# Kernel optimization log

Hardware: AMD Instinct MI355X
Metric: run time of the kernel (lower is better)

## Reference

```python
import jax, jax.numpy as jnp
import numpy as np

HEADS = 8
EMBED = 512


def setup_inputs() -> dict:
    key = jax.random.key(0)
    ks = jax.random.split(key, 9)
    N, KL, QL, S = 4, 512, 32, 64
    D = EMBED // HEADS
    return {
        "values": jax.random.normal(ks[0], (N, KL, EMBED), jnp.float32),
        "keys": jax.random.normal(ks[1], (N, KL, EMBED), jnp.float32),
        "query": jax.random.normal(ks[2], (N, QL, S, EMBED), jnp.float32),
        "mask": jax.random.randint(ks[3], (N, 1, 1, KL, 1), 0, 2, jnp.int32),
        "Wv": jax.random.normal(ks[4], (D, D), jnp.float32) * 0.05,
        "Wk": jax.random.normal(ks[5], (D, D), jnp.float32) * 0.05,
        "Wq": jax.random.normal(ks[6], (D, D), jnp.float32) * 0.05,
        "Wo": jax.random.normal(ks[7], (EMBED, EMBED), jnp.float32) * 0.05,
        "bo": jax.random.normal(ks[8], (EMBED,), jnp.float32) * 0.05,
    }


def reference(values, keys, query, mask, Wv, Wk, Wq, Wo, bo):
    N, KL, E = keys.shape
    QL, S = query.shape[1], query.shape[2]
    H = HEADS
    D = E // H
    # split heads, then per-head linear (weights shared across heads, torch y = x @ W.T)
    v = jnp.einsum('nkhd,ed->nkhe', values.reshape(N, KL, H, D), Wv)
    k = jnp.einsum('nkhd,ed->nkhe', keys.reshape(N, KL, H, D), Wk)
    q = jnp.einsum('nqshd,ed->nqshe', query.reshape(N, QL, S, H, D), Wq)
    # energy: [N, H, QL, KL, S]
    energy = jnp.einsum('nqshd,nkhd->nhqks', q, k)
    energy = jnp.where(mask == 0, jnp.float32(-1e20), energy)
    scale = jnp.float32(E ** 0.5)
    attention = jax.nn.softmax(energy / scale, axis=3)  # softmax over key axis
    out = jnp.einsum('nhqks,nkhd->nqshd', attention, v).reshape(N, QL, S, E)
    return out @ Wo.T + bo
```

## Files before the change

kernel.cpp:

```cpp
#include <hip/hip_runtime.h>
#include <math.h>


typedef __bf16 bf16;
typedef __attribute__((ext_vector_type(8))) __bf16 bf16x8;
typedef __attribute__((ext_vector_type(4))) __bf16 bf16x4;
typedef __attribute__((ext_vector_type(4))) float f32x4;

#define LA 72
#define QSCALE (0.044194173824159216f * 1.4426950408889634f)
#define MASK_BIAS -64.0f

__global__ __launch_bounds__(256) void wcvt(const float* __restrict__ Wq,
                                            const float* __restrict__ Wk,
                                            const float* __restrict__ Wv,
                                            const float* __restrict__ Wo,
                                            bf16* __restrict__ Wq_bf,
                                            bf16* __restrict__ Wk_bf,
                                            bf16* __restrict__ Wv_bf,
                                            bf16* __restrict__ Wo_bf) {
    int t = blockIdx.x * 256 + threadIdx.x;
    if (t < 262144) Wo_bf[t] = (bf16)Wo[t];
    if (t < 4096) {
        Wq_bf[t] = (bf16)(Wq[t] * QSCALE);
        Wk_bf[t] = (bf16)Wk[t];
        Wv_bf[t] = (bf16)Wv[t];
    }
}

__global__ __launch_bounds__(128, 2) void kv_proj(const float* __restrict__ keys,
                                                  const float* __restrict__ values,
                                                  const bf16* __restrict__ Wk_bf,
                                                  const bf16* __restrict__ Wv_bf,
                                                  bf16* __restrict__ Kp,
                                                  bf16* __restrict__ Vt) {
    __shared__ bf16 Xk[64 * LA];
    __shared__ bf16 Xv[64 * LA];
    int t = threadIdx.x;
    int nh = blockIdx.x >> 3, kt = blockIdx.x & 7;
    int n = nh >> 3, h = nh & 7;
    int kl0 = kt * 64;
#pragma unroll
    for (int i = 0; i < 8; ++i) {
        int f = t + i * 128;
        int row = f >> 4, c4 = f & 15;
        float4 a = *(const float4*)(keys + ((long)n * 512 + kl0 + row) * 512 + h * 64 + c4 * 4);
        float4 b = *(const float4*)(values + ((long)n * 512 + kl0 + row) * 512 + h * 64 + c4 * 4);
        bf16x4 ak = {(bf16)a.x, (bf16)a.y, (bf16)a.z, (bf16)a.w};
        bf16x4 bv = {(bf16)b.x, (bf16)b.y, (bf16)b.z, (bf16)b.w};
        *(bf16x4*)&Xk[row * LA + c4 * 4] = ak;
        *(bf16x4*)&Xv[row * LA + c4 * 4] = bv;
    }
    __syncthreads();
    int w = t >> 6, quad = (t >> 4) & 3, c16 = t & 15;
    {
        f32x4 acc[2][4];
#pragma unroll
        for (int mb = 0; mb < 2; ++mb)
#pragma unroll
            for (int nb = 0; nb < 4; ++nb) acc[mb][nb] = (f32x4){0.f, 0.f, 0.f, 0.f};
#pragma unroll
        for (int kc = 0; kc < 2; ++kc) {
            bf16x8 a0 = *(const bf16x8*)&Xk[(32 * w + c16) * LA + 32 * kc + quad * 8];
            bf16x8 a1 = *(const bf16x8*)&Xk[(32 * w + 16 + c16) * LA + 32 * kc + quad * 8];
#pragma unroll
            for (int nb = 0; nb < 4; ++nb) {
                bf16x8 b = *(const bf16x8*)(Wk_bf + (16 * nb + c16) * 64 + 32 * kc + quad * 8);
                acc[0][nb] = __builtin_amdgcn_mfma_f32_16x16x32_bf16(a0, b, acc[0][nb], 0, 0, 0);
                acc[1][nb] = __builtin_amdgcn_mfma_f32_16x16x32_bf16(a1, b, acc[1][nb], 0, 0, 0);
            }
        }
#pragma unroll
        for (int mb = 0; mb < 2; ++mb)
#pragma unroll
            for (int nb = 0; nb < 4; ++nb)
#pragma unroll
                for (int r = 0; r < 4; ++r)
                    Kp[((long)nh * 512 + kl0 + 32 * w + 16 * mb + quad * 4 + r) * 64 + 16 * nb + c16] =
                        (bf16)acc[mb][nb][r];
    }
    {
        f32x4 acc[2][4];
#pragma unroll
        for (int mb = 0; mb < 2; ++mb)
#pragma unroll
            for (int nb = 0; nb < 4; ++nb) acc[mb][nb] = (f32x4){0.f, 0.f, 0.f, 0.f};
#pragma unroll
        for (int kc = 0; kc < 2; ++kc) {
            bf16x8 a0 = *(const bf16x8*)(Wv_bf + (32 * w + c16) * 64 + 32 * kc + quad * 8);
            bf16x8 a1 = *(const bf16x8*)(Wv_bf + (32 * w + 16 + c16) * 64 + 32 * kc + quad * 8);
#pragma unroll
            for (int nb = 0; nb < 4; ++nb) {
                bf16x8 b = *(const bf16x8*)&Xv[(16 * nb + c16) * LA + 32 * kc + quad * 8];
                acc[0][nb] = __builtin_amdgcn_mfma_f32_16x16x32_bf16(a0, b, acc[0][nb], 0, 0, 0);
                acc[1][nb] = __builtin_amdgcn_mfma_f32_16x16x32_bf16(a1, b, acc[1][nb], 0, 0, 0);
            }
        }
#pragma unroll
        for (int mb = 0; mb < 2; ++mb)
#pragma unroll
            for (int nb = 0; nb < 4; ++nb)
#pragma unroll
                for (int r = 0; r < 4; ++r)
                    Vt[((long)nh * 64 + 32 * w + 16 * mb + quad * 4 + r) * 512 + kl0 + 16 * nb + c16] =
                        (bf16)acc[mb][nb][r];
    }
}

__global__ __launch_bounds__(256, 2) void attn(const float* __restrict__ query,
                                               const bf16* __restrict__ Wq_bf,
                                               const bf16* __restrict__ Kp,
                                               const bf16* __restrict__ Vtg,
                                               const int* __restrict__ mask,
                                               bf16* __restrict__ AO) {
    __shared__ bf16 Xq[128 * LA];
    __shared__ bf16 Qt[128 * LA];
    __shared__ bf16 Kt[64 * LA];
    __shared__ bf16 Vs[64 * LA];
    __shared__ bf16 St[128 * LA];
    __shared__ float Mb[64];
    int t = threadIdx.x;
    int qt = blockIdx.x & 15;
    int nh = blockIdx.x >> 4;
    int n = nh >> 3, h = nh & 7;
    int r0 = qt * 128;
    int w = t >> 6, quad = (t >> 4) & 3, c16 = t & 15;

#pragma unroll
    for (int i = 0; i < 8; ++i) {
        int f = t + i * 256;
        int row = f >> 4, c4 = f & 15;
        float4 a = *(const float4*)(query + ((long)n * 2048 + r0 + row) * 512 + h * 64 + c4 * 4);
        bf16x4 v = {(bf16)a.x, (bf16)a.y, (bf16)a.z, (bf16)a.w};
        *(bf16x4*)&Xq[row * LA + c4 * 4] = v;
    }
    __syncthreads();
    {
        f32x4 qa[2][4];
#pragma unroll
        for (int mb = 0; mb < 2; ++mb)
#pragma unroll
            for (int nb = 0; nb < 4; ++nb) qa[mb][nb] = (f32x4){0.f, 0.f, 0.f, 0.f};
#pragma unroll
        for (int kc = 0; kc < 2; ++kc) {
            bf16x8 a0 = *(const bf16x8*)&Xq[(32 * w + c16) * LA + 32 * kc + quad * 8];
            bf16x8 a1 = *(const bf16x8*)&Xq[(32 * w + 16 + c16) * LA + 32 * kc + quad * 8];
#pragma unroll
            for (int nb = 0; nb < 4; ++nb) {
                bf16x8 b = *(const bf16x8*)(Wq_bf + (16 * nb + c16) * 64 + 32 * kc + quad * 8);
                qa[0][nb] = __builtin_amdgcn_mfma_f32_16x16x32_bf16(a0, b, qa[0][nb], 0, 0, 0);
                qa[1][nb] = __builtin_amdgcn_mfma_f32_16x16x32_bf16(a1, b, qa[1][nb], 0, 0, 0);
            }
        }
#pragma unroll
        for (int mb = 0; mb < 2; ++mb)
#pragma unroll
            for (int nb = 0; nb < 4; ++nb)
#pragma unroll
                for (int r = 0; r < 4; ++r)
                    Qt[(32 * w + 16 * mb + quad * 4 + r) * LA + 16 * nb + c16] = (bf16)qa[mb][nb][r];
    }

    f32x4 oacc[4][2];
#pragma unroll
    for (int mb = 0; mb < 4; ++mb)
#pragma unroll
        for (int nb = 0; nb < 2; ++nb) oacc[mb][nb] = (f32x4){0.f, 0.f, 0.f, 0.f};
    float ps[2] = {0.f, 0.f};
    const bf16* Kb = Kp + (long)nh * 512 * 64;
    const bf16* Vb = Vtg + (long)nh * 64 * 512;

    for (int kt = 0; kt < 8; ++kt) {
        __syncthreads();
#pragma unroll
        for (int i = 0; i < 2; ++i) {
            int f = t + i * 256;
            int row = f >> 3, c = f & 7;
            *(bf16x8*)&Kt[row * LA + c * 8] = *(const bf16x8*)(Kb + ((long)kt * 64 + row) * 64 + c * 8);
            *(bf16x8*)&Vs[row * LA + c * 8] = *(const bf16x8*)(Vb + (long)row * 512 + kt * 64 + c * 8);
        }
        if (t < 64) Mb[t] = mask[n * 512 + kt * 64 + t] ? 0.f : MASK_BIAS;
        __syncthreads();
        f32x4 sc[4][2];
#pragma unroll
        for (int mb = 0; mb < 4; ++mb) {
            f32x4 bias = *(const f32x4*)&Mb[16 * mb + quad * 4];
            sc[mb][0] = bias;
            sc[mb][1] = bias;
        }
#pragma unroll
        for (int kc = 0; kc < 2; ++kc) {
            bf16x8 ka[4];
#pragma unroll
            for (int mb = 0; mb < 4; ++mb)
                ka[mb] = *(const bf16x8*)&Kt[(16 * mb + c16) * LA + 32 * kc + quad * 8];
#pragma unroll
            for (int nb = 0; nb < 2; ++nb) {
                bf16x8 qb = *(const bf16x8*)&Qt[(32 * w + 16 * nb + c16) * LA + 32 * kc + quad * 8];
#pragma unroll
                for (int mb = 0; mb < 4; ++mb)
                    sc[mb][nb] = __builtin_amdgcn_mfma_f32_16x16x32_bf16(ka[mb], qb, sc[mb][nb], 0, 0, 0);
            }
        }
#pragma unroll
        for (int mb = 0; mb < 4; ++mb)
#pragma unroll
            for (int nb = 0; nb < 2; ++nb) {
                float p0 = exp2f(sc[mb][nb][0]);
                float p1 = exp2f(sc[mb][nb][1]);
                float p2 = exp2f(sc[mb][nb][2]);
                float p3 = exp2f(sc[mb][nb][3]);
                ps[nb] += (p0 + p1) + (p2 + p3);
                bf16x4 pb = {(bf16)p0, (bf16)p1, (bf16)p2, (bf16)p3};
                *(bf16x4*)&St[(32 * w + 16 * nb + c16) * LA + 16 * mb + quad * 4] = pb;
            }
#pragma unroll
        for (int kc = 0; kc < 2; ++kc) {
            bf16x8 va[4];
#pragma unroll
            for (int mb = 0; mb < 4; ++mb)
                va[mb] = *(const bf16x8*)&Vs[(16 * mb + c16) * LA + 32 * kc + quad * 8];
#pragma unroll
            for (int nb = 0; nb < 2; ++nb) {
                bf16x8 pb = *(const bf16x8*)&St[(32 * w + 16 * nb + c16) * LA + 32 * kc + quad * 8];
#pragma unroll
                for (int mb = 0; mb < 4; ++mb)
                    oacc[mb][nb] = __builtin_amdgcn_mfma_f32_16x16x32_bf16(va[mb], pb, oacc[mb][nb], 0, 0, 0);
            }
        }
    }
#pragma unroll
    for (int nb = 0; nb < 2; ++nb) {
        ps[nb] += __shfl_xor(ps[nb], 16);
        ps[nb] += __shfl_xor(ps[nb], 32);
    }
    float il[2] = {1.0f / ps[0], 1.0f / ps[1]};
#pragma unroll
    for (int mb = 0; mb < 4; ++mb)
#pragma unroll
        for (int nb = 0; nb < 2; ++nb) {
            int row_g = r0 + 32 * w + 16 * nb + c16;
            int d = 16 * mb + quad * 4;
            bf16x4 o = {(bf16)(oacc[mb][nb][0] * il[nb]), (bf16)(oacc[mb][nb][1] * il[nb]),
                        (bf16)(oacc[mb][nb][2] * il[nb]), (bf16)(oacc[mb][nb][3] * il[nb])};
            *(bf16x4*)(AO + ((long)n * 2048 + row_g) * 512 + h * 64 + d) = o;
        }
}

__global__ __launch_bounds__(256, 2) void out_gemm(const bf16* __restrict__ A,
                                                   const bf16* __restrict__ Wo_bf,
                                                   const float* __restrict__ bo,
                                                   float* __restrict__ C) {
    __shared__ bf16 At[128 * LA];
    __shared__ bf16 Bt[64 * LA];
    int t = threadIdx.x;
    int br = blockIdx.x >> 3, bc = blockIdx.x & 7;
    int r0 = br * 128, c0 = bc * 64;
    int w = t >> 6, quad = (t >> 4) & 3, c16 = t & 15;
    f32x4 acc[2][4];
#pragma unroll
    for (int mb = 0; mb < 2; ++mb)
#pragma unroll
        for (int nb = 0; nb < 4; ++nb) acc[mb][nb] = (f32x4){0.f, 0.f, 0.f, 0.f};
    for (int k0 = 0; k0 < 512; k0 += 64) {
        __syncthreads();
#pragma unroll
        for (int i = 0; i < 4; ++i) {
            int f = t + i * 256;
            int row = f >> 3, c = f & 7;
            *(bf16x8*)&At[row * LA + c * 8] = *(const bf16x8*)(A + (long)(r0 + row) * 512 + k0 + c * 8);
        }
#pragma unroll
        for (int i = 0; i < 2; ++i) {
            int f = t + i * 256;
            int row = f >> 3, c = f & 7;
            *(bf16x8*)&Bt[row * LA + c * 8] = *(const bf16x8*)(Wo_bf + (long)(c0 + row) * 512 + k0 + c * 8);
        }
        __syncthreads();
#pragma unroll
        for (int kc = 0; kc < 2; ++kc) {
            bf16x8 a0 = *(const bf16x8*)&At[(32 * w + c16) * LA + 32 * kc + quad * 8];
            bf16x8 a1 = *(const bf16x8*)&At[(32 * w + 16 + c16) * LA + 32 * kc + quad * 8];
#pragma unroll
            for (int nb = 0; nb < 4; ++nb) {
                bf16x8 b = *(const bf16x8*)&Bt[(16 * nb + c16) * LA + 32 * kc + quad * 8];
                acc[0][nb] = __builtin_amdgcn_mfma_f32_16x16x32_bf16(a0, b, acc[0][nb], 0, 0, 0);
                acc[1][nb] = __builtin_amdgcn_mfma_f32_16x16x32_bf16(a1, b, acc[1][nb], 0, 0, 0);
            }
        }
    }
#pragma unroll
    for (int mb = 0; mb < 2; ++mb)
#pragma unroll
        for (int nb = 0; nb < 4; ++nb) {
            float bias = bo[c0 + 16 * nb + c16];
#pragma unroll
            for (int r = 0; r < 4; ++r)
                C[(long)(r0 + 32 * w + 16 * mb + quad * 4 + r) * 512 + c0 + 16 * nb + c16] =
                    acc[mb][nb][r] + bias;
        }
}

extern "C" void kernel_launch(void* const* d_in, const int* in_sizes, int n_in,
                              void* d_out, int out_size, void* d_ws, size_t ws_size,
                              hipStream_t stream) {
    const float* values = (const float*)d_in[0];
    const float* keys   = (const float*)d_in[1];
    const float* query  = (const float*)d_in[2];
    const int*   maskp  = (const int*)d_in[3];
    const float* Wv     = (const float*)d_in[4];
    const float* Wk     = (const float*)d_in[5];
    const float* Wq     = (const float*)d_in[6];
    const float* Wo     = (const float*)d_in[7];
    const float* bo     = (const float*)d_in[8];
    float* out = (float*)d_out;

    bf16* ws = (bf16*)d_ws;
    bf16* Kp    = ws;
    bf16* Vt    = Kp + 1048576;
    bf16* AO    = Vt + 1048576;
    bf16* Wq_bf = AO + 4194304;
    bf16* Wk_bf = Wq_bf + 4096;
    bf16* Wv_bf = Wk_bf + 4096;
    bf16* Wo_bf = Wv_bf + 4096;

    wcvt<<<dim3(1024), dim3(256), 0, stream>>>(Wq, Wk, Wv, Wo, Wq_bf, Wk_bf, Wv_bf, Wo_bf);
    kv_proj<<<dim3(256), dim3(128), 0, stream>>>(keys, values, Wk_bf, Wv_bf, Kp, Vt);
    attn<<<dim3(512), dim3(256), 0, stream>>>(query, Wq_bf, Kp, Vt, maskp, AO);
    out_gemm<<<dim3(512), dim3(256), 0, stream>>>(AO, Wo_bf, bo, out);
}
```

Before: 127.5 us.

## Drop weight-conversion kernel, prefetch K/V tiles, reuse LDS, remap block order

The separate weight-conversion launch is removed. Each kernel now converts its fp32 weights to bf16 in registers, and Wq is scaled on load. kv_proj uses 256 threads so the K and V projections run on separate warps in parallel. attn and out_gemm prefetch the next K/V/mask or A/Wo tile into registers while the current tile is computed. attn also shares one LDS buffer between Xq and the probability tile, lowers padding to 68 and raises occupancy to 3 blocks. Block index orderings change for L2 locality, in exchange for redundant weight conversion in every block and more register pressure.

Measured after the change: 126.0 us. Within noise of the previous version (-1.2%).

```diff
diff --git a/kernel.cpp b/kernel.cpp
--- a/kernel.cpp
+++ b/kernel.cpp
@@ -7,53 +7,47 @@
 typedef __attribute__((ext_vector_type(4))) __bf16 bf16x4;
 typedef __attribute__((ext_vector_type(4))) float f32x4;
 
-#define LA 72
+#define LW 68
+#define LS 72
 #define QSCALE (0.044194173824159216f * 1.4426950408889634f)
 #define MASK_BIAS -64.0f
 
-__global__ __launch_bounds__(256) void wcvt(const float* __restrict__ Wq,
-                                            const float* __restrict__ Wk,
-                                            const float* __restrict__ Wv,
-                                            const float* __restrict__ Wo,
-                                            bf16* __restrict__ Wq_bf,
-                                            bf16* __restrict__ Wk_bf,
-                                            bf16* __restrict__ Wv_bf,
-                                            bf16* __restrict__ Wo_bf) {
-    int t = blockIdx.x * 256 + threadIdx.x;
-    if (t < 262144) Wo_bf[t] = (bf16)Wo[t];
-    if (t < 4096) {
-        Wq_bf[t] = (bf16)(Wq[t] * QSCALE);
-        Wk_bf[t] = (bf16)Wk[t];
-        Wv_bf[t] = (bf16)Wv[t];
-    }
-}
-
-__global__ __launch_bounds__(128, 2) void kv_proj(const float* __restrict__ keys,
+__device__ __forceinline__ bf16x8 cvt8(const float* p, float s) {
+    float4 x0 = *(const float4*)p;
+    float4 x1 = *(const float4*)(p + 4);
+    bf16x8 r = {(bf16)(x0.x * s), (bf16)(x0.y * s), (bf16)(x0.z * s), (bf16)(x0.w * s),
+                (bf16)(x1.x * s), (bf16)(x1.y * s), (bf16)(x1.z * s), (bf16)(x1.w * s)};
+    return r;
+}
+
+__global__ __launch_bounds__(256, 2) void kv_proj(const float* __restrict__ keys,
                                                   const float* __restrict__ values,
-                                                  const bf16* __restrict__ Wk_bf,
-                                                  const bf16* __restrict__ Wv_bf,
+                                                  const float* __restrict__ Wk,
+                                                  const float* __restrict__ Wv,
                                                   bf16* __restrict__ Kp,
                                                   bf16* __restrict__ Vt) {
-    __shared__ bf16 Xk[64 * LA];
-    __shared__ bf16 Xv[64 * LA];
+    __shared__ bf16 Xk[64 * LW];
+    __shared__ bf16 Xv[64 * LW];
     int t = threadIdx.x;
     int nh = blockIdx.x >> 3, kt = blockIdx.x & 7;
-    int n = nh >> 3, h = nh & 7;
-    int kl0 = kt * 64;
-#pragma unroll
-    for (int i = 0; i < 8; ++i) {
-        int f = t + i * 128;
-        int row = f >> 4, c4 = f & 15;
+    int n = nh >> 3, h = nh & 7, kl0 = kt * 64;
+    int w = t >> 6, quad = (t >> 4) & 3, c16 = t & 15;
+#pragma unroll
+    for (int i = 0; i < 4; ++i) {
+        int f = t + i * 256, row = f >> 4, c4 = f & 15;
         float4 a = *(const float4*)(keys + ((long)n * 512 + kl0 + row) * 512 + h * 64 + c4 * 4);
         float4 b = *(const float4*)(values + ((long)n * 512 + kl0 + row) * 512 + h * 64 + c4 * 4);
-        bf16x4 ak = {(bf16)a.x, (bf16)a.y, (bf16)a.z, (bf16)a.w};
-        bf16x4 bv = {(bf16)b.x, (bf16)b.y, (bf16)b.z, (bf16)b.w};
-        *(bf16x4*)&Xk[row * LA + c4 * 4] = ak;
-        *(bf16x4*)&Xv[row * LA + c4 * 4] = bv;
+        *(bf16x4*)&Xk[row * LW + c4 * 4] = (bf16x4){(bf16)a.x, (bf16)a.y, (bf16)a.z, (bf16)a.w};
+        *(bf16x4*)&Xv[row * LW + c4 * 4] = (bf16x4){(bf16)b.x, (bf16)b.y, (bf16)b.z, (bf16)b.w};
     }
     __syncthreads();
-    int w = t >> 6, quad = (t >> 4) & 3, c16 = t & 15;
-    {
+    if (w < 2) {
+        bf16x8 wf[8];
+#pragma unroll
+        for (int nb = 0; nb < 4; ++nb)
+#pragma unroll
+            for (int kc = 0; kc < 2; ++kc)
+                wf[nb * 2 + kc] = cvt8(Wk + (16 * nb + c16) * 64 + 32 * kc + quad * 8, 1.0f);
         f32x4 acc[2][4];
 #pragma unroll
         for (int mb = 0; mb < 2; ++mb)
@@ -61,13 +55,12 @@
             for (int nb = 0; nb < 4; ++nb) acc[mb][nb] = (f32x4){0.f, 0.f, 0.f, 0.f};
 #pragma unroll
         for (int kc = 0; kc < 2; ++kc) {
-            bf16x8 a0 = *(const bf16x8*)&Xk[(32 * w + c16) * LA + 32 * kc + quad * 8];
-            bf16x8 a1 = *(const bf16x8*)&Xk[(32 * w + 16 + c16) * LA + 32 * kc + quad * 8];
+            bf16x8 a0 = *(const bf16x8*)&Xk[(32 * w + c16) * LW + 32 * kc + quad * 8];
+            bf16x8 a1 = *(const bf16x8*)&Xk[(32 * w + 16 + c16) * LW + 32 * kc + quad * 8];
 #pragma unroll
             for (int nb = 0; nb < 4; ++nb) {
-                bf16x8 b = *(const bf16x8*)(Wk_bf + (16 * nb + c16) * 64 + 32 * kc + quad * 8);
-                acc[0][nb] = __builtin_amdgcn_mfma_f32_16x16x32_bf16(a0, b, acc[0][nb], 0, 0, 0);
-                acc[1][nb] = __builtin_amdgcn_mfma_f32_16x16x32_bf16(a1, b, acc[1][nb], 0, 0, 0);
+                acc[0][nb] = __builtin_amdgcn_mfma_f32_16x16x32_bf16(a0, wf[nb * 2 + kc], acc[0][nb], 0, 0, 0);
+                acc[1][nb] = __builtin_amdgcn_mfma_f32_16x16x32_bf16(a1, wf[nb * 2 + kc], acc[1][nb], 0, 0, 0);
             }
         }
 #pragma unroll
@@ -78,8 +71,14 @@
                 for (int r = 0; r < 4; ++r)
                     Kp[((long)nh * 512 + kl0 + 32 * w + 16 * mb + quad * 4 + r) * 64 + 16 * nb + c16] =
                         (bf16)acc[mb][nb][r];
-    }
-    {
+    } else {
+        int w2 = w - 2;
+        bf16x8 af[4];
+#pragma unroll
+        for (int mb = 0; mb < 2; ++mb)
+#pragma unroll
+            for (int kc = 0; kc < 2; ++kc)
+                af[mb * 2 + kc] = cvt8(Wv + (32 * w2 + 16 * mb + c16) * 64 + 32 * kc + quad * 8, 1.0f);
         f32x4 acc[2][4];
 #pragma unroll
         for (int mb = 0; mb < 2; ++mb)
@@ -87,13 +86,11 @@
             for (int nb = 0; nb < 4; ++nb) acc[mb][nb] = (f32x4){0.f, 0.f, 0.f, 0.f};
 #pragma unroll
         for (int kc = 0; kc < 2; ++kc) {
-            bf16x8 a0 = *(const bf16x8*)(Wv_bf + (32 * w + c16) * 64 + 32 * kc + quad * 8);
-            bf16x8 a1 = *(const bf16x8*)(Wv_bf + (32 * w + 16 + c16) * 64 + 32 * kc + quad * 8);
 #pragma unroll
             for (int nb = 0; nb < 4; ++nb) {
-                bf16x8 b = *(const bf16x8*)&Xv[(16 * nb + c16) * LA + 32 * kc + quad * 8];
-                acc[0][nb] = __builtin_amdgcn_mfma_f32_16x16x32_bf16(a0, b, acc[0][nb], 0, 0, 0);
-                acc[1][nb] = __builtin_amdgcn_mfma_f32_16x16x32_bf16(a1, b, acc[1][nb], 0, 0, 0);
+                bf16x8 b = *(const bf16x8*)&Xv[(16 * nb + c16) * LW + 32 * kc + quad * 8];
+                acc[0][nb] = __builtin_amdgcn_mfma_f32_16x16x32_bf16(af[kc], b, acc[0][nb], 0, 0, 0);
+                acc[1][nb] = __builtin_amdgcn_mfma_f32_16x16x32_bf16(af[2 + kc], b, acc[1][nb], 0, 0, 0);
             }
         }
 #pragma unroll
@@ -102,37 +99,51 @@
             for (int nb = 0; nb < 4; ++nb)
 #pragma unroll
                 for (int r = 0; r < 4; ++r)
-                    Vt[((long)nh * 64 + 32 * w + 16 * mb + quad * 4 + r) * 512 + kl0 + 16 * nb + c16] =
+                    Vt[((long)nh * 64 + 32 * w2 + 16 * mb + quad * 4 + r) * 512 + kl0 + 16 * nb + c16] =
                         (bf16)acc[mb][nb][r];
     }
 }
 
-__global__ __launch_bounds__(256, 2) void attn(const float* __restrict__ query,
-                                               const bf16* __restrict__ Wq_bf,
+__global__ __launch_bounds__(256, 3) void attn(const float* __restrict__ query,
+                                               const float* __restrict__ Wq,
                                                const bf16* __restrict__ Kp,
                                                const bf16* __restrict__ Vtg,
                                                const int* __restrict__ mask,
                                                bf16* __restrict__ AO) {
-    __shared__ bf16 Xq[128 * LA];
-    __shared__ bf16 Qt[128 * LA];
-    __shared__ bf16 Kt[64 * LA];
-    __shared__ bf16 Vs[64 * LA];
-    __shared__ bf16 St[128 * LA];
+    __shared__ bf16 SX[128 * LS];
+    __shared__ bf16 Qt[128 * LW];
+    __shared__ bf16 Kt[64 * LW];
+    __shared__ bf16 Vs[64 * LW];
     __shared__ float Mb[64];
     int t = threadIdx.x;
-    int qt = blockIdx.x & 15;
-    int nh = blockIdx.x >> 4;
+    int nh = blockIdx.x & 31, qtile = blockIdx.x >> 5;
     int n = nh >> 3, h = nh & 7;
-    int r0 = qt * 128;
+    int r0 = qtile * 128;
     int w = t >> 6, quad = (t >> 4) & 3, c16 = t & 15;
+    const bf16* Kb = Kp + (long)nh * 512 * 64;
+    const bf16* Vb = Vtg + (long)nh * 64 * 512;
+
+    int prow0 = t >> 3, pcol0 = t & 7;
+    int prow1 = (t + 256) >> 3, pcol1 = t & 7;
+    bf16x8 pk0 = *(const bf16x8*)(Kb + (long)prow0 * 64 + pcol0 * 8);
+    bf16x8 pk1 = *(const bf16x8*)(Kb + (long)prow1 * 64 + pcol1 * 8);
+    bf16x8 pv0 = *(const bf16x8*)(Vb + (long)prow0 * 512 + pcol0 * 8);
+    bf16x8 pv1 = *(const bf16x8*)(Vb + (long)prow1 * 512 + pcol1 * 8);
+    float mnext = 0.f;
+    if (t < 64) mnext = mask[n * 512 + t] ? 0.f : MASK_BIAS;
+
+    bf16x8 wf[8];
+#pragma unroll
+    for (int nb = 0; nb < 4; ++nb)
+#pragma unroll
+        for (int kc = 0; kc < 2; ++kc)
+            wf[nb * 2 + kc] = cvt8(Wq + (16 * nb + c16) * 64 + 32 * kc + quad * 8, QSCALE);
 
 #pragma unroll
     for (int i = 0; i < 8; ++i) {
-        int f = t + i * 256;
-        int row = f >> 4, c4 = f & 15;
+        int f = t + i * 256, row = f >> 4, c4 = f & 15;
         float4 a = *(const float4*)(query + ((long)n * 2048 + r0 + row) * 512 + h * 64 + c4 * 4);
-        bf16x4 v = {(bf16)a.x, (bf16)a.y, (bf16)a.z, (bf16)a.w};
-        *(bf16x4*)&Xq[row * LA + c4 * 4] = v;
+        *(bf16x4*)&SX[row * LS + c4 * 4] = (bf16x4){(bf16)a.x, (bf16)a.y, (bf16)a.z, (bf16)a.w};
     }
     __syncthreads();
     {
@@ -143,13 +154,12 @@
             for (int nb = 0; nb < 4; ++nb) qa[mb][nb] = (f32x4){0.f, 0.f, 0.f, 0.f};
 #pragma unroll
         for (int kc = 0; kc < 2; ++kc) {
-            bf16x8 a0 = *(const bf16x8*)&Xq[(32 * w + c16) * LA + 32 * kc + quad * 8];
-            bf16x8 a1 = *(const bf16x8*)&Xq[(32 * w + 16 + c16) * LA + 32 * kc + quad * 8];
+            bf16x8 a0 = *(const bf16x8*)&SX[(32 * w + c16) * LS + 32 * kc + quad * 8];
+            bf16x8 a1 = *(const bf16x8*)&SX[(32 * w + 16 + c16) * LS + 32 * kc + quad * 8];
 #pragma unroll
             for (int nb = 0; nb < 4; ++nb) {
-                bf16x8 b = *(const bf16x8*)(Wq_bf + (16 * nb + c16) * 64 + 32 * kc + quad * 8);
-                qa[0][nb] = __builtin_amdgcn_mfma_f32_16x16x32_bf16(a0, b, qa[0][nb], 0, 0, 0);
-                qa[1][nb] = __builtin_amdgcn_mfma_f32_16x16x32_bf16(a1, b, qa[1][nb], 0, 0, 0);
+                qa[0][nb] = __builtin_amdgcn_mfma_f32_16x16x32_bf16(a0, wf[nb * 2 + kc], qa[0][nb], 0, 0, 0);
+                qa[1][nb] = __builtin_amdgcn_mfma_f32_16x16x32_bf16(a1, wf[nb * 2 + kc], qa[1][nb], 0, 0, 0);
             }
         }
 #pragma unroll
@@ -158,7 +168,7 @@
             for (int nb = 0; nb < 4; ++nb)
 #pragma unroll
                 for (int r = 0; r < 4; ++r)
-                    Qt[(32 * w + 16 * mb + quad * 4 + r) * LA + 16 * nb + c16] = (bf16)qa[mb][nb][r];
+                    Qt[(32 * w + 16 * mb + quad * 4 + r) * LW + 16 * nb + c16] = (bf16)qa[mb][nb][r];
     }
 
     f32x4 oacc[4][2];
@@ -167,20 +177,24 @@
 #pragma unroll
         for (int nb = 0; nb < 2; ++nb) oacc[mb][nb] = (f32x4){0.f, 0.f, 0.f, 0.f};
     float ps[2] = {0.f, 0.f};
-    const bf16* Kb = Kp + (long)nh * 512 * 64;
-    const bf16* Vb = Vtg + (long)nh * 64 * 512;
 
     for (int kt = 0; kt < 8; ++kt) {
+        if (kt) __syncthreads();
+        *(bf16x8*)&Kt[prow0 * LW + pcol0 * 8] = pk0;
+        *(bf16x8*)&Kt[prow1 * LW + pcol1 * 8] = pk1;
+        *(bf16x8*)&Vs[prow0 * LW + pcol0 * 8] = pv0;
+        *(bf16x8*)&Vs[prow1 * LW + pcol1 * 8] = pv1;
+        if (t < 64) Mb[t] = mnext;
         __syncthreads();
-#pragma unroll
-        for (int i = 0; i < 2; ++i) {
-            int f = t + i * 256;
-            int row = f >> 3, c = f & 7;
-            *(bf16x8*)&Kt[row * LA + c * 8] = *(const bf16x8*)(Kb + ((long)kt * 64 + row) * 64 + c * 8);
-            *(bf16x8*)&Vs[row * LA + c * 8] = *(const bf16x8*)(Vb + (long)row * 512 + kt * 64 + c * 8);
-        }
-        if (t < 64) Mb[t] = mask[n * 512 + kt * 64 + t] ? 0.f : MASK_BIAS;
-        __syncthreads();
+        if (kt < 7) {
+            const bf16* Kn = Kb + (long)(kt + 1) * 64 * 64;
+            const bf16* Vn = Vb + (kt + 1) * 64;
+            pk0 = *(const bf16x8*)(Kn + (long)prow0 * 64 + pcol0 * 8);
+            pk1 = *(const bf16x8*)(Kn + (long)prow1 * 64 + pcol1 * 8);
+            pv0 = *(const bf16x8*)(Vn + (long)prow0 * 512 + pcol0 * 8);
+            pv1 = *(const bf16x8*)(Vn + (long)prow1 * 512 + pcol1 * 8);
+            if (t < 64) mnext = mask[n * 512 + (kt + 1) * 64 + t] ? 0.f : MASK_BIAS;
+        }
         f32x4 sc[4][2];
 #pragma unroll
         for (int mb = 0; mb < 4; ++mb) {
@@ -193,10 +207,10 @@
             bf16x8 ka[4];
 #pragma unroll
             for (int mb = 0; mb < 4; ++mb)
-                ka[mb] = *(const bf16x8*)&Kt[(16 * mb + c16) * LA + 32 * kc + quad * 8];
+                ka[mb] = *(const bf16x8*)&Kt[(16 * mb + c16) * LW + 32 * kc + quad * 8];
 #pragma unroll
             for (int nb = 0; nb < 2; ++nb) {
-                bf16x8 qb = *(const bf16x8*)&Qt[(32 * w + 16 * nb + c16) * LA + 32 * kc + quad * 8];
+                bf16x8 qb = *(const bf16x8*)&Qt[(32 * w + 16 * nb + c16) * LW + 32 * kc + quad * 8];
 #pragma unroll
                 for (int mb = 0; mb < 4; ++mb)
                     sc[mb][nb] = __builtin_amdgcn_mfma_f32_16x16x32_bf16(ka[mb], qb, sc[mb][nb], 0, 0, 0);
@@ -211,18 +225,18 @@
                 float p2 = exp2f(sc[mb][nb][2]);
                 float p3 = exp2f(sc[mb][nb][3]);
                 ps[nb] += (p0 + p1) + (p2 + p3);
-                bf16x4 pb = {(bf16)p0, (bf16)p1, (bf16)p2, (bf16)p3};
-                *(bf16x4*)&St[(32 * w + 16 * nb + c16) * LA + 16 * mb + quad * 4] = pb;
+                *(bf16x4*)&SX[(32 * w + 16 * nb + c16) * LS + 16 * mb + quad * 4] =
+                    (bf16x4){(bf16)p0, (bf16)p1, (bf16)p2, (bf16)p3};
             }
 #pragma unroll
         for (int kc = 0; kc < 2; ++kc) {
             bf16x8 va[4];
 #pragma unroll
             for (int mb = 0; mb < 4; ++mb)
-                va[mb] = *(const bf16x8*)&Vs[(16 * mb + c16) * LA + 32 * kc + quad * 8];
+                va[mb] = *(const bf16x8*)&Vs[(16 * mb + c16) * LW + 32 * kc + quad * 8];
 #pragma unroll
             for (int nb = 0; nb < 2; ++nb) {
-                bf16x8 pb = *(const bf16x8*)&St[(32 * w + 16 * nb + c16) * LA + 32 * kc + quad * 8];
+                bf16x8 pb = *(const bf16x8*)&SX[(32 * w + 16 * nb + c16) * LS + 32 * kc + quad * 8];
 #pragma unroll
                 for (int mb = 0; mb < 4; ++mb)
                     oacc[mb][nb] = __builtin_amdgcn_mfma_f32_16x16x32_bf16(va[mb], pb, oacc[mb][nb], 0, 0, 0);
@@ -240,50 +254,71 @@
 #pragma unroll
         for (int nb = 0; nb < 2; ++nb) {
             int row_g = r0 + 32 * w + 16 * nb + c16;
-            int d = 16 * mb + quad * 4;
-            bf16x4 o = {(bf16)(oacc[mb][nb][0] * il[nb]), (bf16)(oacc[mb][nb][1] * il[nb]),
-                        (bf16)(oacc[mb][nb][2] * il[nb]), (bf16)(oacc[mb][nb][3] * il[nb])};
-            *(bf16x4*)(AO + ((long)n * 2048 + row_g) * 512 + h * 64 + d) = o;
+            *(bf16x4*)(AO + ((long)n * 2048 + row_g) * 512 + h * 64 + 16 * mb + quad * 4) =
+                (bf16x4){(bf16)(oacc[mb][nb][0] * il[nb]), (bf16)(oacc[mb][nb][1] * il[nb]),
+                         (bf16)(oacc[mb][nb][2] * il[nb]), (bf16)(oacc[mb][nb][3] * il[nb])};
         }
 }
 
 __global__ __launch_bounds__(256, 2) void out_gemm(const bf16* __restrict__ A,
-                                                   const bf16* __restrict__ Wo_bf,
+                                                   const float* __restrict__ Wo,
                                                    const float* __restrict__ bo,
                                                    float* __restrict__ C) {
-    __shared__ bf16 At[128 * LA];
-    __shared__ bf16 Bt[64 * LA];
+    __shared__ bf16 At[128 * LW];
+    __shared__ bf16 Bt[64 * LW];
     int t = threadIdx.x;
-    int br = blockIdx.x >> 3, bc = blockIdx.x & 7;
+    int br = blockIdx.x & 63, bc = blockIdx.x >> 6;
     int r0 = br * 128, c0 = bc * 64;
     int w = t >> 6, quad = (t >> 4) & 3, c16 = t & 15;
+    int arow[4], acol[4];
+#pragma unroll
+    for (int i = 0; i < 4; ++i) {
+        int f = t + i * 256;
+        arow[i] = f >> 3;
+        acol[i] = f & 7;
+    }
+    int wrow[4], wcol[4];
+#pragma unroll
+    for (int i = 0; i < 4; ++i) {
+        int f = t + i * 256;
+        wrow[i] = f >> 4;
+        wcol[i] = f & 15;
+    }
+    bf16x8 pa[4];
+    float4 pw[4];
+#pragma unroll
+    for (int i = 0; i < 4; ++i) {
+        pa[i] = *(const bf16x8*)(A + (long)(r0 + arow[i]) * 512 + acol[i] * 8);
+        pw[i] = *(const float4*)(Wo + (long)(c0 + wrow[i]) * 512 + wcol[i] * 4);
+    }
     f32x4 acc[2][4];
 #pragma unroll
     for (int mb = 0; mb < 2; ++mb)
 #pragma unroll
         for (int nb = 0; nb < 4; ++nb) acc[mb][nb] = (f32x4){0.f, 0.f, 0.f, 0.f};
     for (int k0 = 0; k0 < 512; k0 += 64) {
+        if (k0) __syncthreads();
+#pragma unroll
+        for (int i = 0; i < 4; ++i) {
+            *(bf16x8*)&At[arow[i] * LW + acol[i] * 8] = pa[i];
+            *(bf16x4*)&Bt[wrow[i] * LW + wcol[i] * 4] =
+                (bf16x4){(bf16)pw[i].x, (bf16)pw[i].y, (bf16)pw[i].z, (bf16)pw[i].w};
+        }
         __syncthreads();
-#pragma unroll
-        for (int i = 0; i < 4; ++i) {
-            int f = t + i * 256;
-            int row = f >> 3, c = f & 7;
-            *(bf16x8*)&At[row * LA + c * 8] = *(const bf16x8*)(A + (long)(r0 + row) * 512 + k0 + c * 8);
-        }
-#pragma unroll
-        for (int i = 0; i < 2; ++i) {
-            int f = t + i * 256;
-            int row = f >> 3, c = f & 7;
-            *(bf16x8*)&Bt[row * LA + c * 8] = *(const bf16x8*)(Wo_bf + (long)(c0 + row) * 512 + k0 + c * 8);
-        }
-        __syncthreads();
-#pragma unroll
-        for (int kc = 0; kc < 2; ++kc) {
-            bf16x8 a0 = *(const bf16x8*)&At[(32 * w + c16) * LA + 32 * kc + quad * 8];
-            bf16x8 a1 = *(const bf16x8*)&At[(32 * w + 16 + c16) * LA + 32 * kc + quad * 8];
+        if (k0 < 448) {
+#pragma unroll
+            for (int i = 0; i < 4; ++i) {
+                pa[i] = *(const bf16x8*)(A + (long)(r0 + arow[i]) * 512 + k0 + 64 + acol[i] * 8);
+                pw[i] = *(const float4*)(Wo + (long)(c0 + wrow[i]) * 512 + k0 + 64 + wcol[i] * 4);
+            }
+        }
+#pragma unroll
+        for (int kc = 0; kc < 2; ++kc) {
+            bf16x8 a0 = *(const bf16x8*)&At[(32 * w + c16) * LW + 32 * kc + quad * 8];
+            bf16x8 a1 = *(const bf16x8*)&At[(32 * w + 16 + c16) * LW + 32 * kc + quad * 8];
 #pragma unroll
             for (int nb = 0; nb < 4; ++nb) {
-                bf16x8 b = *(const bf16x8*)&Bt[(16 * nb + c16) * LA + 32 * kc + quad * 8];
+                bf16x8 b = *(const bf16x8*)&Bt[(16 * nb + c16) * LW + 32 * kc + quad * 8];
                 acc[0][nb] = __builtin_amdgcn_mfma_f32_16x16x32_bf16(a0, b, acc[0][nb], 0, 0, 0);
                 acc[1][nb] = __builtin_amdgcn_mfma_f32_16x16x32_bf16(a1, b, acc[1][nb], 0, 0, 0);
             }
@@ -316,16 +351,11 @@
     float* out = (float*)d_out;
 
     bf16* ws = (bf16*)d_ws;
-    bf16* Kp    = ws;
-    bf16* Vt    = Kp + 1048576;
-    bf16* AO    = Vt + 1048576;
-    bf16* Wq_bf = AO + 4194304;
-    bf16* Wk_bf = Wq_bf + 4096;
-    bf16* Wv_bf = Wk_bf + 4096;
-    bf16* Wo_bf = Wv_bf + 4096;
-
-    wcvt<<<dim3(1024), dim3(256), 0, stream>>>(Wq, Wk, Wv, Wo, Wq_bf, Wk_bf, Wv_bf, Wo_bf);
-    kv_proj<<<dim3(256), dim3(128), 0, stream>>>(keys, values, Wk_bf, Wv_bf, Kp, Vt);
-    attn<<<dim3(512), dim3(256), 0, stream>>>(query, Wq_bf, Kp, Vt, maskp, AO);
-    out_gemm<<<dim3(512), dim3(256), 0, stream>>>(AO, Wo_bf, bo, out);
-}
+    bf16* Kp = ws;
+    bf16* Vt = Kp + 1048576;
+    bf16* AO = Vt + 1048576;
+
+    kv_proj<<<dim3(256), dim3(256), 0, stream>>>(keys, values, Wk, Wv, Kp, Vt);
+    attn<<<dim3(512), dim3(256), 0, stream>>>(query, Wq, Kp, Vt, maskp, AO);
+    out_gemm<<<dim3(512), dim3(256), 0, stream>>>(AO, Wo, bo, out);
+}
```
